# Performance work log

Hardware: AMD Instinct MI355X
Metric: run time of the kernel (lower is better)

## Reference

```python
import jax, jax.numpy as jnp
import numpy as np

D_MODEL = 768
NUM_HEADS = 12
HEAD_DIM = D_MODEL // NUM_HEADS

def setup_inputs() -> dict:
    key = jax.random.key(0)
    ks = jax.random.split(key, 7)
    B, S = 2, 4096
    q = jax.random.normal(ks[0], (B, S, D_MODEL), dtype=jnp.float32)
    k = jax.random.normal(ks[1], (B, S, D_MODEL), dtype=jnp.float32)
    v = jax.random.normal(ks[2], (B, S, D_MODEL), dtype=jnp.float32)
    # nn.Linear(d, d, bias=False): weight [out, in], y = x @ W.T
    s = 1.0 / np.sqrt(D_MODEL)
    W_q = jax.random.uniform(ks[3], (D_MODEL, D_MODEL), jnp.float32, -s, s)
    W_k = jax.random.uniform(ks[4], (D_MODEL, D_MODEL), jnp.float32, -s, s)
    W_v = jax.random.uniform(ks[5], (D_MODEL, D_MODEL), jnp.float32, -s, s)
    W_o = jax.random.uniform(ks[6], (D_MODEL, D_MODEL), jnp.float32, -s, s)
    return {"query": q, "key": k, "value": v,
            "W_q": W_q, "W_k": W_k, "W_v": W_v, "W_o": W_o}

def reference(query, key, value, W_q, W_k, W_v, W_o):
    B, S, _ = query.shape
    H, Dh = NUM_HEADS, HEAD_DIM
    scale = np.sqrt(Dh).astype(np.float32)

    def proj(x, W):  # x [B,S,D] -> [B,H,S,Dh]
        y = jnp.einsum('bsd,ed->bse', x, W)
        return y.reshape(B, S, H, Dh).transpose(0, 2, 1, 3)

    Q = proj(query, W_q)
    K = proj(key, W_k)
    V = proj(value, W_v)
    scores = jnp.einsum('bhqd,bhkd->bhqk', Q, K) / scale
    attn = jax.nn.softmax(scores, axis=-1)  # dropout p=0 -> identity (eval)
    out = jnp.einsum('bhqk,bhkd->bhqd', attn, V)
    out = out.transpose(0, 2, 1, 3).reshape(B, S, H * Dh)
    return jnp.einsum('bsd,ed->bse', out, W_o)
```

## Files before the change

### kernel.cpp

```cpp
#include <hip/hip_runtime.h>

#define D_MODEL 768
#define S_LEN   4096
#define NHEAD   12
#define HDIM    64
#define BATCH   2
#define M_ROWS  (BATCH * S_LEN)

typedef __bf16    bf16x8 __attribute__((ext_vector_type(8)));
typedef float     f32x4  __attribute__((ext_vector_type(4)));
typedef float     f32x16 __attribute__((ext_vector_type(16)));
typedef unsigned  u32x4  __attribute__((ext_vector_type(4)));

#define QSCALE 0.18033688011f

__device__ __forceinline__ unsigned int bfb(float x) {
    return (unsigned int)__builtin_bit_cast(unsigned short, (__bf16)x);
}

__device__ __forceinline__ unsigned cvtpk(float lo, float hi) {
    unsigned r;
    asm("v_cvt_pk_bf16_f32 %0, %1, %2" : "=v"(r) : "v"(lo), "v"(hi));
    return r;
}

#if !__has_builtin(__builtin_amdgcn_exp2f)
extern "C" __device__ float __ocml_native_exp2_f32(float);
#endif
__device__ __forceinline__ float fexp2(float x) {
#if __has_builtin(__builtin_amdgcn_exp2f)
    return __builtin_amdgcn_exp2f(x);
#else
    return __ocml_native_exp2_f32(x);
#endif
}

__device__ __forceinline__ void gload16(const void* g, const void* l) {
    __builtin_amdgcn_global_load_lds(
        (const __attribute__((address_space(1))) unsigned int*)g,
        (__attribute__((address_space(3))) unsigned int*)l, 16, 0, 0);
}

#define MFMA16(a, b, c) __builtin_amdgcn_mfma_f32_16x16x32_bf16(a, b, c, 0, 0, 0)
#define MFMA32(a, b, c) __builtin_amdgcn_mfma_f32_32x32x16_bf16(a, b, c, 0, 0, 0)

__global__ __launch_bounds__(256)
void cvt_bf16(const float* __restrict__ s0, const float* __restrict__ s1,
              const float* __restrict__ s2, const float* __restrict__ s3,
              __bf16* __restrict__ d0, __bf16* __restrict__ d1,
              __bf16* __restrict__ d2, __bf16* __restrict__ d3, int n) {
    const int z = blockIdx.y;
    const float* s = z == 0 ? s0 : z == 1 ? s1 : z == 2 ? s2 : s3;
    __bf16*      d = z == 0 ? d0 : z == 1 ? d1 : z == 2 ? d2 : d3;
    const size_t i = ((size_t)blockIdx.x * 256 + threadIdx.x) * 8;
    if (i >= (size_t)n) return;
    float4 a = *(const float4*)(s + i);
    float4 b = *(const float4*)(s + i + 4);
    bf16x8 o;
    o[0] = (__bf16)a.x; o[1] = (__bf16)a.y; o[2] = (__bf16)a.z; o[3] = (__bf16)a.w;
    o[4] = (__bf16)b.x; o[5] = (__bf16)b.y; o[6] = (__bf16)b.z; o[7] = (__bf16)b.w;
    *(bf16x8*)(d + i) = o;
}

__global__ __launch_bounds__(256)
void mm_qkv(const __bf16* __restrict__ X0, const __bf16* __restrict__ X1,
            const __bf16* __restrict__ X2, const __bf16* __restrict__ W0,
            const __bf16* __restrict__ W1, const __bf16* __restrict__ W2,
            __bf16* __restrict__ C0q, __bf16* __restrict__ C1k,
            __bf16* __restrict__ C2v) {
    __shared__ __align__(16) char lds[12288];
    const int z = blockIdx.z;
    const __bf16* Xb = z == 0 ? X0 : z == 1 ? X1 : X2;
    const __bf16* Wb = z == 0 ? W0 : z == 1 ? W1 : W2;

    const int t    = threadIdx.x;
    const int w    = t >> 6;
    const int wr   = w >> 1, wc = w & 1;
    const int lane = t & 63;
    const int q15  = lane & 15;
    const int g    = lane >> 4;
    const int n0   = blockIdx.x * 64;
    const int m0   = blockIdx.y * 128;

    f32x4 acc[4][2];
#pragma unroll
    for (int i = 0; i < 4; i++)
#pragma unroll
        for (int j = 0; j < 2; j++) acc[i][j] = (f32x4){0.f, 0.f, 0.f, 0.f};

    const int srow  = lane >> 2;
    const int sslot = lane & 3;

    for (int k0 = 0; k0 < D_MODEL; k0 += 32) {
        __syncthreads();
#pragma unroll
        for (int j = 0; j < 2; j++) {
            const int lrow = j * 64 + w * 16 + srow;
            const int xs   = (lrow ^ (lrow >> 2)) & 3;
            gload16(Xb + (size_t)(m0 + lrow) * D_MODEL + k0 + ((sslot ^ xs) << 3),
                    lds + j * 4096 + w * 1024);
        }
        {
            const int lrow = w * 16 + srow;
            const int xs   = (lrow ^ (lrow >> 2)) & 3;
            gload16(Wb + (size_t)(n0 + lrow) * D_MODEL + k0 + ((sslot ^ xs) << 3),
                    lds + 8192 + w * 1024);
        }
        __syncthreads();

        bf16x8 xa[4], wf[2];
#pragma unroll
        for (int mi = 0; mi < 4; mi++) {
            const int r  = wr * 64 + mi * 16 + q15;
            const int sl = g ^ ((r ^ (r >> 2)) & 3);
            xa[mi] = *(const bf16x8*)(lds + r * 64 + sl * 16);
        }
#pragma unroll
        for (int nj = 0; nj < 2; nj++) {
            const int r  = wc * 32 + nj * 16 + q15;
            const int sl = g ^ ((r ^ (r >> 2)) & 3);
            wf[nj] = *(const bf16x8*)(lds + 8192 + r * 64 + sl * 16);
        }
#pragma unroll
        for (int mi = 0; mi < 4; mi++)
#pragma unroll
            for (int nj = 0; nj < 2; nj++)
                acc[mi][nj] = MFMA16(xa[mi], wf[nj], acc[mi][nj]);
    }

#pragma unroll
    for (int mi = 0; mi < 4; mi++) {
#pragma unroll
        for (int nj = 0; nj < 2; nj++) {
            const int n  = n0 + wc * 32 + nj * 16 + q15;
            const int mb = m0 + wr * 64 + mi * 16 + 4 * g;
            const int h = n >> 6, dh = n & 63;
            if (z == 0) {
#pragma unroll
                for (int r = 0; r < 4; r++) {
                    const int m = mb + r, b = m >> 12, s = m & 4095;
                    C0q[(((size_t)(b * NHEAD + h)) * S_LEN + s) * HDIM + dh] =
                        (__bf16)(acc[mi][nj][r] * QSCALE);
                }
            } else if (z == 1) {
#pragma unroll
                for (int r = 0; r < 4; r++) {
                    const int m = mb + r, b = m >> 12, s = m & 4095;
                    C1k[(((size_t)(b * NHEAD + h)) * S_LEN + s) * HDIM + dh] =
                        (__bf16)acc[mi][nj][r];
                }
            } else {
                const int b = mb >> 12, s = mb & 4095;
                uint2 pk;
                pk.x = bfb(acc[mi][nj][0]) | (bfb(acc[mi][nj][1]) << 16);
                pk.y = bfb(acc[mi][nj][2]) | (bfb(acc[mi][nj][3]) << 16);
                *(uint2*)(C2v +
                    (((size_t)(b * NHEAD + h)) * HDIM + dh) * S_LEN + s) = pk;
            }
        }
    }
}

__global__ __launch_bounds__(256)
void mm_out(const __bf16* __restrict__ Xb, const __bf16* __restrict__ Wb,
            float* __restrict__ C0) {
    __shared__ __align__(16) char lds[12288];
    const int t    = threadIdx.x;
    const int w    = t >> 6;
    const int wr   = w >> 1, wc = w & 1;
    const int lane = t & 63;
    const int q15  = lane & 15;
    const int g    = lane >> 4;
    const int n0   = blockIdx.x * 64;
    const int m0   = blockIdx.y * 128;

    f32x4 acc[4][2];
#pragma unroll
    for (int i = 0; i < 4; i++)
#pragma unroll
        for (int j = 0; j < 2; j++) acc[i][j] = (f32x4){0.f, 0.f, 0.f, 0.f};

    const int srow  = lane >> 2;
    const int sslot = lane & 3;

    for (int k0 = 0; k0 < D_MODEL; k0 += 32) {
        __syncthreads();
#pragma unroll
        for (int j = 0; j < 2; j++) {
            const int lrow = j * 64 + w * 16 + srow;
            const int xs   = (lrow ^ (lrow >> 2)) & 3;
            gload16(Xb + (size_t)(m0 + lrow) * D_MODEL + k0 + ((sslot ^ xs) << 3),
                    lds + j * 4096 + w * 1024);
        }
        {
            const int lrow = w * 16 + srow;
            const int xs   = (lrow ^ (lrow >> 2)) & 3;
            gload16(Wb + (size_t)(n0 + lrow) * D_MODEL + k0 + ((sslot ^ xs) << 3),
                    lds + 8192 + w * 1024);
        }
        __syncthreads();

        bf16x8 xa[4], wf[2];
#pragma unroll
        for (int mi = 0; mi < 4; mi++) {
            const int r  = wr * 64 + mi * 16 + q15;
            const int sl = g ^ ((r ^ (r >> 2)) & 3);
            xa[mi] = *(const bf16x8*)(lds + r * 64 + sl * 16);
        }
#pragma unroll
        for (int nj = 0; nj < 2; nj++) {
            const int r  = wc * 32 + nj * 16 + q15;
            const int sl = g ^ ((r ^ (r >> 2)) & 3);
            wf[nj] = *(const bf16x8*)(lds + 8192 + r * 64 + sl * 16);
        }
#pragma unroll
        for (int mi = 0; mi < 4; mi++)
#pragma unroll
            for (int nj = 0; nj < 2; nj++)
                acc[mi][nj] = MFMA16(xa[mi], wf[nj], acc[mi][nj]);
    }

#pragma unroll
    for (int mi = 0; mi < 4; mi++)
#pragma unroll
        for (int nj = 0; nj < 2; nj++) {
            const int n  = n0 + wc * 32 + nj * 16 + q15;
            const int mb = m0 + wr * 64 + mi * 16 + 4 * g;
#pragma unroll
            for (int r = 0; r < 4; r++)
                C0[(size_t)(mb + r) * D_MODEL + n] = acc[mi][nj][r];
        }
}

__global__ __launch_bounds__(256, 2)
void flash_attn(const __bf16* __restrict__ Qb, const char* __restrict__ Kb,
                const char* __restrict__ Vtb, __bf16* __restrict__ Ab) {
    __shared__ __align__(16) char lds[32768];
    const int t    = threadIdx.x;
    const int w    = t >> 6;
    const int lane = t & 63;
    const int q31  = lane & 31;
    const int hl   = lane >> 5;
    const int swz  = (q31 & 7) << 4;

    const int bid = blockIdx.x;
    const int sb  = (bid & 7) * 96 + (bid >> 3);
    const int bh  = sb >> 5;
    const int qi  = sb & 31;
    const int b   = bh / NHEAD, h = bh % NHEAD;
    const int q0  = qi * 128 + w * 32;

    const char* kbase = Kb  + (size_t)bh * (S_LEN * HDIM * 2);
    const char* vbase = Vtb + (size_t)bh * (HDIM * S_LEN * 2);

    bf16x8 qf[4];
#pragma unroll
    for (int kc = 0; kc < 4; kc++)
        qf[kc] = *(const bf16x8*)(Qb +
            ((size_t)bh * S_LEN + q0 + q31) * HDIM + kc * 16 + hl * 8);

    const bf16x8 onesv = __builtin_bit_cast(bf16x8,
        (u32x4){0x3F803F80u, 0x3F803F80u, 0x3F803F80u, 0x3F803F80u});

    f32x16 o[2], ol;
#pragma unroll
    for (int mt = 0; mt < 2; mt++)
#pragma unroll
        for (int r = 0; r < 16; r++) o[mt][r] = 0.f;
#pragma unroll
    for (int r = 0; r < 16; r++) ol[r] = 0.f;

    const int crow = lane >> 3;
    const int scb  = ((lane & 7) << 4) ^ (crow << 4);

#define STAGE(BASE, KT)                                                        \
    {                                                                          \
        _Pragma("unroll")                                                      \
        for (int j = 0; j < 2; j++) {                                          \
            const int c = 2 * w + j;                                           \
            gload16(kbase + (size_t)((KT) * 64 + c * 8 + crow) * 128 + scb,    \
                    (BASE) + c * 1024);                                        \
            gload16(vbase + (size_t)(c * 8 + crow) * (S_LEN * 2) +             \
                        (size_t)(KT) * 128 + scb,                              \
                    (BASE) + 8192 + c * 1024);                                 \
        }                                                                      \
    }

#define COMPUTE(BASE)                                                          \
    {                                                                          \
        const char* Kt = (BASE);                                               \
        const char* Vt = (BASE) + 8192;                                        \
        f32x16 sA[2];                                                          \
        _Pragma("unroll")                                                      \
        for (int mt = 0; mt < 2; mt++)                                         \
            _Pragma("unroll")                                                  \
            for (int r = 0; r < 16; r++) sA[mt][r] = 0.f;                      \
        __builtin_amdgcn_s_setprio(1);                                         \
        _Pragma("unroll")                                                      \
        for (int kc = 0; kc < 4; kc++) {                                       \
            bf16x8 kf0 = *(const bf16x8*)(Kt + q31 * 128 +                     \
                                          ((32 * kc + 16 * hl) ^ swz));        \
            bf16x8 kf1 = *(const bf16x8*)(Kt + (32 + q31) * 128 +              \
                                          ((32 * kc + 16 * hl) ^ swz));        \
            sA[0] = MFMA32(kf0, qf[kc], sA[0]);                                \
            sA[1] = MFMA32(kf1, qf[kc], sA[1]);                                \
        }                                                                      \
        __builtin_amdgcn_s_setprio(0);                                         \
        _Pragma("unroll")                                                      \
        for (int mt = 0; mt < 2; mt++)                                         \
            _Pragma("unroll")                                                  \
            for (int r = 0; r < 16; r++) sA[mt][r] = fexp2(sA[mt][r]);         \
        u32x4 pf[4];                                                           \
        _Pragma("unroll")                                                      \
        for (int mt = 0; mt < 2; mt++)                                         \
            _Pragma("unroll")                                                  \
            for (int kvc = 0; kvc < 2; kvc++) {                                \
                unsigned w0 = cvtpk(sA[mt][8*kvc+0], sA[mt][8*kvc+1]);         \
                unsigned w1 = cvtpk(sA[mt][8*kvc+2], sA[mt][8*kvc+3]);         \
                unsigned w2 = cvtpk(sA[mt][8*kvc+4], sA[mt][8*kvc+5]);         \
                unsigned w3 = cvtpk(sA[mt][8*kvc+6], sA[mt][8*kvc+7]);         \
                asm volatile("v_permlane32_swap_b32 %0, %1"                    \
                             : "+v"(w0), "+v"(w2));                            \
                asm volatile("v_permlane32_swap_b32 %0, %1"                    \
                             : "+v"(w1), "+v"(w3));                            \
                pf[mt * 2 + kvc] = (u32x4){w0, w1, w2, w3};                    \
            }                                                                  \
        __builtin_amdgcn_s_setprio(1);                                         \
        _Pragma("unroll")                                                      \
        for (int ks = 0; ks < 4; ks++)                                         \
            ol = MFMA32(onesv, __builtin_bit_cast(bf16x8, pf[ks]), ol);        \
        _Pragma("unroll")                                                      \
        for (int mtd = 0; mtd < 2; mtd++)                                      \
            _Pragma("unroll")                                                  \
            for (int ks = 0; ks < 4; ks++) {                                   \
                bf16x8 vf = *(const bf16x8*)(Vt + (32 * mtd + q31) * 128 +     \
                                             ((32 * ks + 16 * hl) ^ swz));     \
                o[mtd] = MFMA32(vf,                                            \
                    __builtin_bit_cast(bf16x8, pf[ks]), o[mtd]);               \
            }                                                                  \
        __builtin_amdgcn_s_setprio(0);                                         \
    }

    STAGE(lds, 0);
    __syncthreads();
#pragma unroll 1
    for (int kt = 0; kt < S_LEN / 64; kt += 2) {
        STAGE(lds + 16384, kt + 1);
        COMPUTE(lds);
        __syncthreads();
        if (kt + 2 < S_LEN / 64) STAGE(lds, kt + 2);
        COMPUTE(lds + 16384);
        __syncthreads();
    }
#undef STAGE
#undef COMPUTE

    const float inv  = 1.0f / ol[0];
    const int   qrow = q0 + q31;
    __bf16* orow = Ab + ((size_t)b * S_LEN + qrow) * D_MODEL + h * HDIM;
#pragma unroll
    for (int mtd = 0; mtd < 2; mtd++)
#pragma unroll
        for (int rg = 0; rg < 4; rg++) {
            const int d0 = 32 * mtd + 8 * rg + 4 * hl;
            uint2 pk;
            pk.x = cvtpk(o[mtd][rg * 4 + 0] * inv, o[mtd][rg * 4 + 1] * inv);
            pk.y = cvtpk(o[mtd][rg * 4 + 2] * inv, o[mtd][rg * 4 + 3] * inv);
            *(uint2*)(orow + d0) = pk;
        }
}

extern "C" void kernel_launch(void* const* d_in, const int* in_sizes, int n_in,
                              void* d_out, int out_size, void* d_ws, size_t ws_size,
                              hipStream_t stream) {
    const float* q  = (const float*)d_in[0];
    const float* k  = (const float*)d_in[1];
    const float* v  = (const float*)d_in[2];
    const float* Wq = (const float*)d_in[3];
    const float* Wk = (const float*)d_in[4];
    const float* Wv = (const float*)d_in[5];
    const float* Wo = (const float*)d_in[6];
    float* out = (float*)d_out;

    const size_t per = (size_t)M_ROWS * D_MODEL;
    const size_t wsz = (size_t)D_MODEL * D_MODEL;
    __bf16* ws  = (__bf16*)d_ws;
    __bf16* qb  = ws;
    __bf16* kb  = qb  + per;
    __bf16* vb  = kb  + per;
    __bf16* Wqb = vb  + per;
    __bf16* Wkb = Wqb + wsz;
    __bf16* Wvb = Wkb + wsz;
    __bf16* Wob = Wvb + wsz;
    __bf16* Qhi = Wob + wsz;
    __bf16* Kbb = Qhi + per;
    __bf16* Vtb = Kbb + per;

    cvt_bf16<<<dim3((int)(per / 2048), 3), 256, 0, stream>>>(
        q, k, v, nullptr, qb, kb, vb, nullptr, (int)per);
    cvt_bf16<<<dim3((int)(wsz / 2048), 4), 256, 0, stream>>>(
        Wq, Wk, Wv, Wo, Wqb, Wkb, Wvb, Wob, (int)wsz);

    dim3 mmg(D_MODEL / 64, M_ROWS / 128, 3);
    mm_qkv<<<mmg, 256, 0, stream>>>(qb, kb, vb, Wqb, Wkb, Wvb, Qhi, Kbb, Vtb);

    flash_attn<<<768, 256, 0, stream>>>(Qhi, (const char*)Kbb,
                                        (const char*)Vtb, qb );

    dim3 mmo(D_MODEL / 64, M_ROWS / 128);
    mm_out<<<mmo, 256, 0, stream>>>(qb, Wob, out);
}
```

Baseline: 226.2 us.

## Double-buffer LDS in projection GEMMs to overlap global loads with MFMA

Both the QKV projection GEMM and the output projection GEMM now use two LDS stages. The next K-slice is issued into one buffer while MFMAs consume the other, which cuts the per-iteration sync pairs down to one barrier per stage. The goal is to hide global-to-LDS load latency behind compute. In exchange, LDS use per block doubles to 24KB, which may lower occupancy, and correctness depends on the direct-to-LDS loads completing before the barrier.

Measured after the change: 225.6 us. Within noise of the previous version (-0.3%).

```diff
diff --git a/kernel.cpp b/kernel.cpp
--- a/kernel.cpp
+++ b/kernel.cpp
@@ -68,7 +68,7 @@
             const __bf16* __restrict__ W1, const __bf16* __restrict__ W2,
             __bf16* __restrict__ C0q, __bf16* __restrict__ C1k,
             __bf16* __restrict__ C2v) {
-    __shared__ __align__(16) char lds[12288];
+    __shared__ __align__(16) char lds[24576];
     const int z = blockIdx.z;
     const __bf16* Xb = z == 0 ? X0 : z == 1 ? X1 : X2;
     const __bf16* Wb = z == 0 ? W0 : z == 1 ? W1 : W2;
@@ -91,42 +91,61 @@
     const int srow  = lane >> 2;
     const int sslot = lane & 3;
 
-    for (int k0 = 0; k0 < D_MODEL; k0 += 32) {
-        __syncthreads();
-#pragma unroll
-        for (int j = 0; j < 2; j++) {
-            const int lrow = j * 64 + w * 16 + srow;
-            const int xs   = (lrow ^ (lrow >> 2)) & 3;
-            gload16(Xb + (size_t)(m0 + lrow) * D_MODEL + k0 + ((sslot ^ xs) << 3),
-                    lds + j * 4096 + w * 1024);
-        }
-        {
-            const int lrow = w * 16 + srow;
-            const int xs   = (lrow ^ (lrow >> 2)) & 3;
-            gload16(Wb + (size_t)(n0 + lrow) * D_MODEL + k0 + ((sslot ^ xs) << 3),
-                    lds + 8192 + w * 1024);
-        }
-        __syncthreads();
-
-        bf16x8 xa[4], wf[2];
-#pragma unroll
-        for (int mi = 0; mi < 4; mi++) {
-            const int r  = wr * 64 + mi * 16 + q15;
-            const int sl = g ^ ((r ^ (r >> 2)) & 3);
-            xa[mi] = *(const bf16x8*)(lds + r * 64 + sl * 16);
-        }
-#pragma unroll
-        for (int nj = 0; nj < 2; nj++) {
-            const int r  = wc * 32 + nj * 16 + q15;
-            const int sl = g ^ ((r ^ (r >> 2)) & 3);
-            wf[nj] = *(const bf16x8*)(lds + 8192 + r * 64 + sl * 16);
-        }
-#pragma unroll
-        for (int mi = 0; mi < 4; mi++)
-#pragma unroll
-            for (int nj = 0; nj < 2; nj++)
-                acc[mi][nj] = MFMA16(xa[mi], wf[nj], acc[mi][nj]);
-    }
+#define MM_STAGE(B, K0)                                                        \
+    {                                                                          \
+        _Pragma("unroll")                                                      \
+        for (int j = 0; j < 2; j++) {                                          \
+            const int lrow = j * 64 + w * 16 + srow;                           \
+            const int xs   = (lrow ^ (lrow >> 2)) & 3;                         \
+            gload16(Xb + (size_t)(m0 + lrow) * D_MODEL + (K0) +                \
+                        ((sslot ^ xs) << 3),                                   \
+                    lds + (B) * 12288 + j * 4096 + w * 1024);                  \
+        }                                                                      \
+        {                                                                      \
+            const int lrow = w * 16 + srow;                                    \
+            const int xs   = (lrow ^ (lrow >> 2)) & 3;                         \
+            gload16(Wb + (size_t)(n0 + lrow) * D_MODEL + (K0) +                \
+                        ((sslot ^ xs) << 3),                                   \
+                    lds + (B) * 12288 + 8192 + w * 1024);                      \
+        }                                                                      \
+    }
+
+#define MM_COMPUTE(B)                                                          \
+    {                                                                          \
+        bf16x8 xa[4], wf[2];                                                   \
+        _Pragma("unroll")                                                      \
+        for (int mi = 0; mi < 4; mi++) {                                       \
+            const int r  = wr * 64 + mi * 16 + q15;                            \
+            const int sl = g ^ ((r ^ (r >> 2)) & 3);                           \
+            xa[mi] = *(const bf16x8*)(lds + (B) * 12288 + r * 64 + sl * 16);   \
+        }                                                                      \
+        _Pragma("unroll")                                                      \
+        for (int nj = 0; nj < 2; nj++) {                                       \
+            const int r  = wc * 32 + nj * 16 + q15;                            \
+            const int sl = g ^ ((r ^ (r >> 2)) & 3);                           \
+            wf[nj] = *(const bf16x8*)(lds + (B) * 12288 + 8192 + r * 64 +      \
+                                      sl * 16);                                \
+        }                                                                      \
+        _Pragma("unroll")                                                      \
+        for (int mi = 0; mi < 4; mi++)                                         \
+            _Pragma("unroll")                                                  \
+            for (int nj = 0; nj < 2; nj++)                                     \
+                acc[mi][nj] = MFMA16(xa[mi], wf[nj], acc[mi][nj]);             \
+    }
+
+    MM_STAGE(0, 0);
+    __syncthreads();
+#pragma unroll 1
+    for (int ks = 0; ks < 24; ks += 2) {
+        if (ks + 1 < 24) MM_STAGE(1, (ks + 1) * 32);
+        MM_COMPUTE(0);
+        __syncthreads();
+        if (ks + 2 < 24) MM_STAGE(0, (ks + 2) * 32);
+        MM_COMPUTE(1);
+        __syncthreads();
+    }
+#undef MM_STAGE
+#undef MM_COMPUTE
 
 #pragma unroll
     for (int mi = 0; mi < 4; mi++) {
@@ -164,7 +183,7 @@
 __global__ __launch_bounds__(256)
 void mm_out(const __bf16* __restrict__ Xb, const __bf16* __restrict__ Wb,
             float* __restrict__ C0) {
-    __shared__ __align__(16) char lds[12288];
+    __shared__ __align__(16) char lds[24576];
     const int t    = threadIdx.x;
     const int w    = t >> 6;
     const int wr   = w >> 1, wc = w & 1;
@@ -183,42 +202,61 @@
     const int srow  = lane >> 2;
     const int sslot = lane & 3;
 
-    for (int k0 = 0; k0 < D_MODEL; k0 += 32) {
-        __syncthreads();
-#pragma unroll
-        for (int j = 0; j < 2; j++) {
-            const int lrow = j * 64 + w * 16 + srow;
-            const int xs   = (lrow ^ (lrow >> 2)) & 3;
-            gload16(Xb + (size_t)(m0 + lrow) * D_MODEL + k0 + ((sslot ^ xs) << 3),
-                    lds + j * 4096 + w * 1024);
-        }
-        {
-            const int lrow = w * 16 + srow;
-            const int xs   = (lrow ^ (lrow >> 2)) & 3;
-            gload16(Wb + (size_t)(n0 + lrow) * D_MODEL + k0 + ((sslot ^ xs) << 3),
-                    lds + 8192 + w * 1024);
-        }
-        __syncthreads();
-
-        bf16x8 xa[4], wf[2];
-#pragma unroll
-        for (int mi = 0; mi < 4; mi++) {
-            const int r  = wr * 64 + mi * 16 + q15;
-            const int sl = g ^ ((r ^ (r >> 2)) & 3);
-            xa[mi] = *(const bf16x8*)(lds + r * 64 + sl * 16);
-        }
-#pragma unroll
-        for (int nj = 0; nj < 2; nj++) {
-            const int r  = wc * 32 + nj * 16 + q15;
-            const int sl = g ^ ((r ^ (r >> 2)) & 3);
-            wf[nj] = *(const bf16x8*)(lds + 8192 + r * 64 + sl * 16);
-        }
-#pragma unroll
-        for (int mi = 0; mi < 4; mi++)
-#pragma unroll
-            for (int nj = 0; nj < 2; nj++)
-                acc[mi][nj] = MFMA16(xa[mi], wf[nj], acc[mi][nj]);
-    }
+#define MM_STAGE(B, K0)                                                        \
+    {                                                                          \
+        _Pragma("unroll")                                                      \
+        for (int j = 0; j < 2; j++) {                                          \
+            const int lrow = j * 64 + w * 16 + srow;                           \
+            const int xs   = (lrow ^ (lrow >> 2)) & 3;                         \
+            gload16(Xb + (size_t)(m0 + lrow) * D_MODEL + (K0) +                \
+                        ((sslot ^ xs) << 3),                                   \
+                    lds + (B) * 12288 + j * 4096 + w * 1024);                  \
+        }                                                                      \
+        {                                                                      \
+            const int lrow = w * 16 + srow;                                    \
+            const int xs   = (lrow ^ (lrow >> 2)) & 3;                         \
+            gload16(Wb + (size_t)(n0 + lrow) * D_MODEL + (K0) +                \
+                        ((sslot ^ xs) << 3),                                   \
+                    lds + (B) * 12288 + 8192 + w * 1024);                      \
+        }                                                                      \
+    }
+
+#define MM_COMPUTE(B)                                                          \
+    {                                                                          \
+        bf16x8 xa[4], wf[2];                                                   \
+        _Pragma("unroll")                                                      \
+        for (int mi = 0; mi < 4; mi++) {                                       \
+            const int r  = wr * 64 + mi * 16 + q15;                            \
+            const int sl = g ^ ((r ^ (r >> 2)) & 3);                           \
+            xa[mi] = *(const bf16x8*)(lds + (B) * 12288 + r * 64 + sl * 16);   \
+        }                                                                      \
+        _Pragma("unroll")                                                      \
+        for (int nj = 0; nj < 2; nj++) {                                       \
+            const int r  = wc * 32 + nj * 16 + q15;                            \
+            const int sl = g ^ ((r ^ (r >> 2)) & 3);                           \
+            wf[nj] = *(const bf16x8*)(lds + (B) * 12288 + 8192 + r * 64 +      \
+                                      sl * 16);                                \
+        }                                                                      \
+        _Pragma("unroll")                                                      \
+        for (int mi = 0; mi < 4; mi++)                                         \
+            _Pragma("unroll")                                                  \
+            for (int nj = 0; nj < 2; nj++)                                     \
+                acc[mi][nj] = MFMA16(xa[mi], wf[nj], acc[mi][nj]);             \
+    }
+
+    MM_STAGE(0, 0);
+    __syncthreads();
+#pragma unroll 1
+    for (int ks = 0; ks < 24; ks += 2) {
+        if (ks + 1 < 24) MM_STAGE(1, (ks + 1) * 32);
+        MM_COMPUTE(0);
+        __syncthreads();
+        if (ks + 2 < 24) MM_STAGE(0, (ks + 2) * 32);
+        MM_COMPUTE(1);
+        __syncthreads();
+    }
+#undef MM_STAGE
+#undef MM_COMPUTE
 
 #pragma unroll
     for (int mi = 0; mi < 4; mi++)
```
